# Kernel optimization log

Measured on AMD Instinct MI355X. Metric: run time of the kernel, lower is better.

The kernel has to match this reference:

```python
import jax, jax.numpy as jnp
import numpy as np
from jax import lax

B, L = 2, 5000            # images, candidate lines per image
C_IN, C_LOI = 256, 128    # backbone channels, dim_loi
H = W = 256               # feature-map spatial size (indices clamped to 255)
N_PTS0, N_PTS1 = 32, 8    # points sampled per line, after maxpool
POOL = N_PTS0 // N_PTS1   # MaxPool1d kernel/stride = 4
PLANES = C_LOI // 2       # Bottleneck1D mid channels
EPS = 1e-5


def setup_inputs() -> dict:
    key = jax.random.key(0)
    ks = jax.random.split(key, 16)
    f32 = jnp.float32
    s = 0.05
    feature = jax.random.normal(ks[0], (B, C_IN, H, W), f32)
    lines = jax.random.uniform(ks[1], (B, L, 2, 2), f32, minval=0.0, maxval=255.0)
    return {
        "feature": feature,
        "lines": lines,
        "fc1_w": jax.random.normal(ks[2], (C_LOI, C_IN), f32) * s,
        "fc1_b": jnp.zeros((C_LOI,), f32),
        "bn1_g": jnp.ones((C_LOI,), f32),
        "bn1_b": jnp.zeros((C_LOI,), f32),
        "bn1_m": jax.random.normal(ks[3], (C_LOI,), f32) * 0.1,
        "bn1_v": jax.random.uniform(ks[4], (C_LOI,), f32, minval=0.5, maxval=1.5),
        "conv1_w": jax.random.normal(ks[5], (PLANES, C_LOI), f32) * s,
        "conv1_b": jnp.zeros((PLANES,), f32),
        "bn2_g": jnp.ones((PLANES,), f32),
        "bn2_b": jnp.zeros((PLANES,), f32),
        "bn2_m": jax.random.normal(ks[6], (PLANES,), f32) * 0.1,
        "bn2_v": jax.random.uniform(ks[7], (PLANES,), f32, minval=0.5, maxval=1.5),
        "conv2_w": jax.random.normal(ks[8], (PLANES, PLANES, 3), f32) * s,
        "conv2_b": jnp.zeros((PLANES,), f32),
        "bn3_g": jnp.ones((PLANES,), f32),
        "bn3_b": jnp.zeros((PLANES,), f32),
        "bn3_m": jax.random.normal(ks[9], (PLANES,), f32) * 0.1,
        "bn3_v": jax.random.uniform(ks[10], (PLANES,), f32, minval=0.5, maxval=1.5),
        "conv3_w": jax.random.normal(ks[11], (C_LOI, PLANES), f32) * s,
        "conv3_b": jnp.zeros((C_LOI,), f32),
        "fc2_w": jax.random.normal(ks[12], (3, C_LOI * N_PTS1), f32) * s,
        "fc2_b": jnp.zeros((3,), f32),
    }


def _bn(x, g, b, m, v):
    # eval-mode BatchNorm1d over [N, C, T]
    inv = g / jnp.sqrt(v + EPS)
    return x * inv[None, :, None] + (b - m * inv)[None, :, None]


def _bilinear_sample(feat, lines):
    # feat: [B, C, H, W], lines: [B, L, 2, 2] -> [B, L, C, N_PTS0]
    lam = jnp.linspace(0.0, 1.0, N_PTS0, dtype=feat.dtype)[:, None]  # [P,1]
    # p = lam * endpoint0 + (1-lam) * endpoint1 - 0.5  -> [B, L, P, 2]
    p = lines[:, :, 0:1, :] * lam + lines[:, :, 1:2, :] * (1.0 - lam) - 0.5
    px, py = p[..., 0], p[..., 1]                       # [B, L, P]
    px0 = jnp.clip(jnp.floor(px), 0.0, 255.0)
    py0 = jnp.clip(jnp.floor(py), 0.0, 255.0)
    px1 = jnp.clip(px0 + 1.0, 0.0, 255.0)
    py1 = jnp.clip(py0 + 1.0, 0.0, 255.0)
    ix0, iy0 = px0.astype(jnp.int32), py0.astype(jnp.int32)
    ix1, iy1 = px1.astype(jnp.int32), py1.astype(jnp.int32)
    w00 = (px1 - px) * (py1 - py)
    w10 = (px - px0) * (py1 - py)
    w01 = (px1 - px) * (py - py0)
    w11 = (px - px0) * (py - py0)

    def one_image(f, a0, b0, a1, b1, c00, c10, c01, c11):
        # f: [C,H,W], indices/weights: [L,P] -> [C,L,P]
        return (f[:, a0, b0] * c00 + f[:, a1, b0] * c10 +
                f[:, a0, b1] * c01 + f[:, a1, b1] * c11)

    xp = jax.vmap(one_image)(feat, ix0, iy0, ix1, iy1, w00, w10, w01, w11)
    return jnp.transpose(xp, (0, 2, 1, 3))  # [B, L, C, P]


def _forward(feature, lines, fc1_w, fc1_b, bn1_g, bn1_b, bn1_m, bn1_v,
             conv1_w, conv1_b, bn2_g, bn2_b, bn2_m, bn2_v,
             conv2_w, conv2_b, bn3_g, bn3_b, bn3_m, bn3_v,
             conv3_w, conv3_b, fc2_w, fc2_b):
    # fc1: 1x1 conv over the backbone feature map
    x = jnp.einsum('oc,bchw->bohw', fc1_w, feature) + fc1_b[None, :, None, None]
    xp = _bilinear_sample(x, lines)                     # [B, L, C_LOI, P]
    xp = xp.reshape(B * L, C_LOI, N_PTS0)
    # MaxPool1d(kernel=POOL, stride=POOL)
    xp = xp.reshape(B * L, C_LOI, N_PTS1, POOL).max(axis=-1)  # [N, C, T]
    # Bottleneck1D residual branch: BN-ReLU-Conv1(k1)-BN-ReLU-Conv(k3)-BN-ReLU-Conv(k1)
    h = jax.nn.relu(_bn(xp, bn1_g, bn1_b, bn1_m, bn1_v))
    h = jnp.einsum('oc,nct->not', conv1_w, h) + conv1_b[None, :, None]
    h = jax.nn.relu(_bn(h, bn2_g, bn2_b, bn2_m, bn2_v))
    h = lax.conv_general_dilated(h, conv2_w, window_strides=(1,),
                                 padding=((1, 1),),
                                 dimension_numbers=('NCH', 'OIH', 'NCH'))
    h = h + conv2_b[None, :, None]
    h = jax.nn.relu(_bn(h, bn3_g, bn3_b, bn3_m, bn3_v))
    h = jnp.einsum('oc,nct->not', conv3_w, h) + conv3_b[None, :, None]
    xp = xp + h
    # fc2: ReLU + Linear(dim_loi * n_pts1 -> 3)
    flat = jax.nn.relu(xp).reshape(B * L, C_LOI * N_PTS1)
    return flat @ fc2_w.T + fc2_b


def reference(feature, lines, fc1_w, fc1_b, bn1_g, bn1_b, bn1_m, bn1_v,
              conv1_w, conv1_b, bn2_g, bn2_b, bn2_m, bn2_v,
              conv2_w, conv2_b, bn3_g, bn3_b, bn3_m, bn3_v,
              conv3_w, conv3_b, fc2_w, fc2_b):
    return _forward(feature, lines, fc1_w, fc1_b, bn1_g, bn1_b, bn1_m, bn1_v,
                    conv1_w, conv1_b, bn2_g, bn2_b, bn2_m, bn2_v,
                    conv2_w, conv2_b, bn3_g, bn3_b, bn3_m, bn3_v,
                    conv3_w, conv3_b, fc2_w, fc2_b)
```

## Files before the change

### kernel.cpp

```cpp
#include <hip/hip_runtime.h>
#include <hip/hip_bf16.h>

#define BB 2
#define LL 5000
#define CIN 256
#define CLOI 128
#define HH 256
#define WW 256
#define HWP (HH*WW)
#define NPTS0 32
#define NPTS1 8
#define PLANES 64
#define EPSV 1e-5f

#define X_BYTES   ((size_t)BB * HWP * CLOI * 2)
#define XS_BYTES  ((size_t)BB * LL * 1024 * 2)
#define W1S_OFF   (X_BYTES + XS_BYTES)
#define W2S_OFF   (W1S_OFF + 16384)
#define W3S_OFF   (W2S_OFF + 24576)
#define B1P_OFF   (W3S_OFF + 16384)
#define B2P_OFF   (B1P_OFF + 256)
#define S1_OFF    (B2P_OFF + 256)
#define T1_OFF    (S1_OFF + 512)
#define W0S_OFF   (T1_OFF + 512)

typedef unsigned int uint;
typedef unsigned short ushort;
typedef __attribute__((ext_vector_type(8))) short short8;
typedef __attribute__((ext_vector_type(4))) float f32x4;

__device__ __forceinline__ float bf2f(ushort u) {
    uint v = ((uint)u) << 16;
    return __uint_as_float(v);
}
__device__ __forceinline__ ushort f2bf(float f) {
    uint x = __float_as_uint(f);
    uint r = (x + 0x7fffu + ((x >> 16) & 1u)) >> 16;
    return (ushort)r;
}
__device__ __forceinline__ uint pack2(float a, float b) {
    return (uint)f2bf(a) | ((uint)f2bf(b) << 16);
}

__global__ __launch_bounds__(256) void fc1_kernel(
    const float* __restrict__ feature, const ushort* __restrict__ w0s,
    const float* __restrict__ fc1_b, ushort* __restrict__ xout)
{
    __shared__ ushort sF[32 * 64 * 8];

    int tid = threadIdx.x;
    int tile = blockIdx.x;
    int b = tile >> 10;
    int p0 = (tile & 1023) << 6;
    int wv = tid >> 6, lane = tid & 63;
    int q = lane >> 4, ln = lane & 15;

    short8 afr[8][2];
#pragma unroll
    for (int kg = 0; kg < 8; kg++)
#pragma unroll
        for (int mt = 0; mt < 2; mt++)
            afr[kg][mt] = *(const short8*)(w0s + ((size_t)((kg * 4 + q) * 128 + wv * 32 + mt * 16 + ln)) * 8);

    const float* fb = feature + (size_t)b * CIN * HWP + p0;
    int g_ = tid >> 4;
    int qd = tid & 15;
#pragma unroll
    for (int s = 0; s < 2; s++) {
        int g = s * 16 + g_;
        const float* src = fb + (size_t)(g * 8) * HWP + qd * 4;
        float4 rv[8];
#pragma unroll
        for (int j = 0; j < 8; j++) rv[j] = *(const float4*)(src + (size_t)j * HWP);
#pragma unroll
        for (int i = 0; i < 4; i++) {
            uint4 u;
            u.x = pack2(((const float*)&rv[0])[i], ((const float*)&rv[1])[i]);
            u.y = pack2(((const float*)&rv[2])[i], ((const float*)&rv[3])[i]);
            u.z = pack2(((const float*)&rv[4])[i], ((const float*)&rv[5])[i]);
            u.w = pack2(((const float*)&rv[6])[i], ((const float*)&rv[7])[i]);
            *(uint4*)(&sF[(g * 64 + qd * 4 + i) * 8]) = u;
        }
    }
    __syncthreads();

    const f32x4 fzero = { 0.f, 0.f, 0.f, 0.f };
    f32x4 acc[2][4];
#pragma unroll
    for (int mt = 0; mt < 2; mt++)
#pragma unroll
        for (int nt = 0; nt < 4; nt++) acc[mt][nt] = fzero;

#pragma unroll
    for (int kg = 0; kg < 8; kg++) {
#pragma unroll
        for (int nt = 0; nt < 4; nt++) {
            short8 bfr = *(short8*)(&sF[((kg * 4 + q) * 64 + nt * 16 + ln) * 8]);
            acc[0][nt] = __builtin_amdgcn_mfma_f32_16x16x32_bf16(afr[kg][0], bfr, acc[0][nt], 0, 0, 0);
            acc[1][nt] = __builtin_amdgcn_mfma_f32_16x16x32_bf16(afr[kg][1], bfr, acc[1][nt], 0, 0, 0);
        }
    }

    float bias[8];
    *(float4*)bias       = *(const float4*)(fc1_b + wv * 32 + q * 4);
    *(float4*)(bias + 4) = *(const float4*)(fc1_b + wv * 32 + 16 + q * 4);
    ushort* xrow = xout + (size_t)b * HWP * CLOI;
#pragma unroll
    for (int mt = 0; mt < 2; mt++)
#pragma unroll
        for (int nt = 0; nt < 4; nt++) {
            uint2 u;
            u.x = pack2(acc[mt][nt][0] + bias[mt * 4 + 0], acc[mt][nt][1] + bias[mt * 4 + 1]);
            u.y = pack2(acc[mt][nt][2] + bias[mt * 4 + 2], acc[mt][nt][3] + bias[mt * 4 + 3]);
            *(uint2*)(xrow + (size_t)(p0 + nt * 16 + ln) * CLOI + wv * 32 + mt * 16 + q * 4) = u;
        }
}

__global__ __launch_bounds__(256) void prep_kernel(
    const float* __restrict__ conv1_w, const float* __restrict__ conv1_b,
    const float* __restrict__ bn2_g, const float* __restrict__ bn2_b,
    const float* __restrict__ bn2_m, const float* __restrict__ bn2_v,
    const float* __restrict__ conv2_w, const float* __restrict__ conv2_b,
    const float* __restrict__ bn3_g, const float* __restrict__ bn3_b,
    const float* __restrict__ bn3_m, const float* __restrict__ bn3_v,
    const float* __restrict__ conv3_w,
    const float* __restrict__ bn1_g, const float* __restrict__ bn1_b,
    const float* __restrict__ bn1_m, const float* __restrict__ bn1_v,
    const float* __restrict__ fc1_w,
    ushort* __restrict__ w1s, ushort* __restrict__ w2s, ushort* __restrict__ w3s,
    float* __restrict__ b1p, float* __restrict__ b2p,
    float* __restrict__ s1o, float* __restrict__ t1o,
    ushort* __restrict__ w0s)
{
    int idx = blockIdx.x * 256 + threadIdx.x;
    if (idx < 8192) {
        int kg = idx >> 9, rem = idx & 511, m = rem >> 3, j = rem & 7;
        int c = kg * 8 + j;
        float s2 = bn2_g[m] * rsqrtf(bn2_v[m] + EPSV);
        w1s[idx] = f2bf(conv1_w[m * 128 + c] * s2);
    }
    if (idx < 12288) {
        int dt = idx >> 12, rem = idx & 4095;
        int kg = rem >> 9, m = (rem >> 3) & 63, j = rem & 7;
        int i = kg * 8 + j;
        float s3 = bn3_g[m] * rsqrtf(bn3_v[m] + EPSV);
        w2s[idx] = f2bf(conv2_w[m * 192 + i * 3 + dt] * s3);
    }
    if (idx < 8192) {
        int kg = idx >> 10, rem = idx & 1023, m = rem >> 3, j = rem & 7;
        w3s[idx] = f2bf(conv3_w[m * 64 + kg * 8 + j]);
    }
    if (idx < 32768) {
        int grp = idx >> 10, rem = idx & 1023, m = rem >> 3, j = rem & 7;
        w0s[idx] = f2bf(fc1_w[m * CIN + grp * 8 + j]);
    }
    if (idx < 64) {
        float s2 = bn2_g[idx] * rsqrtf(bn2_v[idx] + EPSV);
        b1p[idx] = conv1_b[idx] * s2 + bn2_b[idx] - bn2_m[idx] * s2;
        float s3 = bn3_g[idx] * rsqrtf(bn3_v[idx] + EPSV);
        b2p[idx] = conv2_b[idx] * s3 + bn3_b[idx] - bn3_m[idx] * s3;
    }
    if (idx < 128) {
        float s1 = bn1_g[idx] * rsqrtf(bn1_v[idx] + EPSV);
        s1o[idx] = s1;
        t1o[idx] = bn1_b[idx] - bn1_m[idx] * s1;
    }
}

__global__ __launch_bounds__(256, 5) void sample_head_kernel(
    const ushort* __restrict__ x, const float* __restrict__ lines,
    const ushort* __restrict__ w1s, const ushort* __restrict__ w2s,
    const ushort* __restrict__ w3s,
    const float* __restrict__ b1p, const float* __restrict__ b2p,
    const float* __restrict__ s1g, const float* __restrict__ t1g,
    const float* __restrict__ conv3_b,
    const float* __restrict__ fc2_w, const float* __restrict__ fc2_b,
    float* __restrict__ out)
{
    __shared__ ushort sH1[8192];
    __shared__ __align__(16) char sU[8192];
    __shared__ float sB1[64], sB2b[64], sB3b[128];

    int*    sI  = (int*)sU;
    float2* sW2 = (float2*)(sU + 1024);
    ushort* sB2 = (ushort*)sU;

    int tid = threadIdx.x;
    int wv = tid >> 6, lane = tid & 63;
    int q = lane >> 4, ln = lane & 15;
    int L0 = blockIdx.x * 8;
    int b = L0 / LL;
    int colg = wv * 16 + ln;

    if (tid < 128) sB3b[tid] = conv3_b[tid];
    if (tid < 64)  { sB1[tid] = b1p[tid]; sB2b[tid] = b2p[tid]; }

    int half = lane >> 5;
    int lc = lane & 31;
    int kg = lc >> 1, j4 = (lc & 1) * 4;
    int swz = (kg & 7) << 3;

    float4 s1v = *(const float4*)(s1g + lc * 4);
    float4 t1v = *(const float4*)(t1g + lc * 4);

    {
        int l = tid >> 5, j = tid & 31;
        float lam = (float)j * (1.0f / 31.0f);
        const float* lp = lines + (size_t)(L0 + l) * 4;
        float e0x = lp[0], e0y = lp[1], e1x = lp[2], e1y = lp[3];
        float px = e0x * lam + e1x * (1.f - lam) - 0.5f;
        float py = e0y * lam + e1y * (1.f - lam) - 0.5f;
        float px0 = fminf(fmaxf(floorf(px), 0.f), 255.f);
        float py0 = fminf(fmaxf(floorf(py), 0.f), 255.f);
        int ix0 = (int)px0, iy0 = (int)py0;
        sI[l * 32 + j] = ix0 * WW + iy0;
        float2 w2; w2.x = px0 + 1.f - px; w2.y = py0 + 1.f - py;
        sW2[l * 32 + j] = w2;
    }
    __syncthreads();

    const uint2* xb2 = (const uint2*)(x + (size_t)b * HWP * CLOI);

    uint2 xsu[8];
#pragma unroll
    for (int l = 0; l < 8; l++) {
        uint2 u[4][4];
        float2 wxy[4];
#pragma unroll
        for (int jj = 0; jj < 4; jj++) {
            int pt = l * 32 + wv * 8 + half * 4 + jj;
            int i00 = sI[pt];
            wxy[jj] = sW2[pt];
            const uint2* rp = xb2 + (size_t)((i00 << 5) + lc);
            u[jj][0] = rp[0];
            u[jj][1] = rp[32];
            u[jj][2] = rp[8192];
            u[jj][3] = rp[8224];
        }
        float p0v = -INFINITY, p1v = -INFINITY, p2v = -INFINITY, p3v = -INFINITY;
#pragma unroll
        for (int jj = 0; jj < 4; jj++) {
            float wx0 = wxy[jj].x, wy0 = wxy[jj].y;
            float w00 = wx0 * wy0;
            float w01 = wx0 - w00;
            float w10 = wy0 - w00;
            float w11 = 1.f - wx0 - wy0 + w00;
            float v0 = bf2f((ushort)(u[jj][0].x & 0xffff)) * w00 + bf2f((ushort)(u[jj][1].x & 0xffff)) * w01
                     + bf2f((ushort)(u[jj][2].x & 0xffff)) * w10 + bf2f((ushort)(u[jj][3].x & 0xffff)) * w11;
            float v1 = bf2f((ushort)(u[jj][0].x >> 16)) * w00 + bf2f((ushort)(u[jj][1].x >> 16)) * w01
                     + bf2f((ushort)(u[jj][2].x >> 16)) * w10 + bf2f((ushort)(u[jj][3].x >> 16)) * w11;
            float v2 = bf2f((ushort)(u[jj][0].y & 0xffff)) * w00 + bf2f((ushort)(u[jj][1].y & 0xffff)) * w01
                     + bf2f((ushort)(u[jj][2].y & 0xffff)) * w10 + bf2f((ushort)(u[jj][3].y & 0xffff)) * w11;
            float v3 = bf2f((ushort)(u[jj][0].y >> 16)) * w00 + bf2f((ushort)(u[jj][1].y >> 16)) * w01
                     + bf2f((ushort)(u[jj][2].y >> 16)) * w10 + bf2f((ushort)(u[jj][3].y >> 16)) * w11;
            p0v = fmaxf(p0v, v0); p1v = fmaxf(p1v, v1);
            p2v = fmaxf(p2v, v2); p3v = fmaxf(p3v, v3);
        }
        uint2 xv; xv.x = pack2(p0v, p1v); xv.y = pack2(p2v, p3v);
        xsu[l] = xv;
        float h0 = fmaxf(p0v * s1v.x + t1v.x, 0.f);
        float h1v = fmaxf(p1v * s1v.y + t1v.y, 0.f);
        float h2 = fmaxf(p2v * s1v.z + t1v.z, 0.f);
        float h3 = fmaxf(p3v * s1v.w + t1v.w, 0.f);
        uint2 hv; hv.x = pack2(h0, h1v); hv.y = pack2(h2, h3);
        int col = l * 8 + 2 * wv + half;
        int base = (kg * 64 + col) * 8 + j4;
        *(uint2*)(&sH1[base ^ swz]) = hv;
    }
    __syncthreads();

    const short8 bzero = { 0, 0, 0, 0, 0, 0, 0, 0 };
    const f32x4 fzero = { 0.f, 0.f, 0.f, 0.f };

    f32x4 acc1[4];
#pragma unroll
    for (int mt = 0; mt < 4; mt++) acc1[mt] = fzero;
#pragma unroll
    for (int ks = 0; ks < 4; ks++) {
        int kk = ks * 4 + q;
        short8 bfrag = *(short8*)(&sH1[((kk * 64 + colg) * 8) ^ ((kk & 7) << 3)]);
#pragma unroll
        for (int mt = 0; mt < 4; mt++) {
            short8 a = *(const short8*)(w1s + (kk * 64 + mt * 16 + ln) * 8);
            acc1[mt] = __builtin_amdgcn_mfma_f32_16x16x32_bf16(a, bfrag, acc1[mt], 0, 0, 0);
        }
    }
#pragma unroll
    for (int mt = 0; mt < 4; mt++) {
        int m0 = mt * 16 + q * 4;
        float v0 = fmaxf(acc1[mt][0] + sB1[m0 + 0], 0.f);
        float v1 = fmaxf(acc1[mt][1] + sB1[m0 + 1], 0.f);
        float v2 = fmaxf(acc1[mt][2] + sB1[m0 + 2], 0.f);
        float v3 = fmaxf(acc1[mt][3] + sB1[m0 + 3], 0.f);
        uint2 u; u.x = pack2(v0, v1); u.y = pack2(v2, v3);
        *(uint2*)(&sB2[((m0 >> 3) * 64 + colg) * 8 + (m0 & 7)]) = u;
    }
    __syncthreads();

#pragma unroll
    for (int l = 0; l < 8; l++) {
        int col = l * 8 + 2 * wv + half;
        int base = (kg * 64 + col) * 8 + j4;
        *(uint2*)(&sH1[base ^ swz]) = xsu[l];
    }

    int tpos = colg & 7;
    short8 bfr2[3][2];
#pragma unroll
    for (int dt = 0; dt < 3; dt++) {
        int tsh = tpos + dt - 1;
        bool valid = ((unsigned)tsh < 8u);
        int colr = colg + dt - 1;
        colr = colr < 0 ? 0 : (colr > 63 ? 63 : colr);
#pragma unroll
        for (int ks = 0; ks < 2; ks++) {
            short8 bfrag = *(short8*)(&sB2[((ks * 4 + q) * 64 + colr) * 8]);
            bfr2[dt][ks] = valid ? bfrag : bzero;
        }
    }
    __syncthreads();

    f32x4 acc2[4];
#pragma unroll
    for (int mt = 0; mt < 4; mt++) acc2[mt] = fzero;
#pragma unroll
    for (int dt = 0; dt < 3; dt++)
#pragma unroll
        for (int ks = 0; ks < 2; ks++) {
            int kk = ks * 4 + q;
#pragma unroll
            for (int mt = 0; mt < 4; mt++) {
                short8 a = *(const short8*)(w2s + dt * 4096 + (kk * 64 + mt * 16 + ln) * 8);
                acc2[mt] = __builtin_amdgcn_mfma_f32_16x16x32_bf16(a, bfr2[dt][ks], acc2[mt], 0, 0, 0);
            }
        }
#pragma unroll
    for (int mt = 0; mt < 4; mt++) {
        int m0 = mt * 16 + q * 4;
        float v0 = fmaxf(acc2[mt][0] + sB2b[m0 + 0], 0.f);
        float v1 = fmaxf(acc2[mt][1] + sB2b[m0 + 1], 0.f);
        float v2 = fmaxf(acc2[mt][2] + sB2b[m0 + 2], 0.f);
        float v3 = fmaxf(acc2[mt][3] + sB2b[m0 + 3], 0.f);
        uint2 u; u.x = pack2(v0, v1); u.y = pack2(v2, v3);
        *(uint2*)(&sB2[((m0 >> 3) * 64 + colg) * 8 + (m0 & 7)]) = u;
    }
    __syncthreads();

    f32x4 acc3[8];
#pragma unroll
    for (int mt = 0; mt < 8; mt++) acc3[mt] = fzero;
#pragma unroll
    for (int ks = 0; ks < 2; ks++) {
        int kk = ks * 4 + q;
        short8 bfrag = *(short8*)(&sB2[(kk * 64 + colg) * 8]);
#pragma unroll
        for (int mt = 0; mt < 8; mt++) {
            short8 a = *(const short8*)(w3s + (kk * 128 + mt * 16 + ln) * 8);
            acc3[mt] = __builtin_amdgcn_mfma_f32_16x16x32_bf16(a, bfrag, acc3[mt], 0, 0, 0);
        }
    }

    float p0 = 0.f, p1 = 0.f, p2 = 0.f;
#pragma unroll
    for (int mt = 0; mt < 8; mt++) {
#pragma unroll
        for (int r = 0; r < 4; r++) {
            int m = mt * 16 + q * 4 + r;
            int idx = ((m >> 3) * 512 + colg * 8 + (m & 7)) ^ (((m >> 3) & 7) << 3);
            float xsv = bf2f(sH1[idx]);
            float v = fmaxf(xsv + acc3[mt][r] + sB3b[m], 0.f);
            int fi = m * 8 + tpos;
            p0 += v * fc2_w[fi];
            p1 += v * fc2_w[1024 + fi];
            p2 += v * fc2_w[2048 + fi];
        }
    }
    p0 += __shfl_xor(p0, 32); p1 += __shfl_xor(p1, 32); p2 += __shfl_xor(p2, 32);
    p0 += __shfl_xor(p0, 16); p1 += __shfl_xor(p1, 16); p2 += __shfl_xor(p2, 16);
    p0 += __shfl_xor(p0, 4);  p1 += __shfl_xor(p1, 4);  p2 += __shfl_xor(p2, 4);
    p0 += __shfl_xor(p0, 2);  p1 += __shfl_xor(p1, 2);  p2 += __shfl_xor(p2, 2);
    p0 += __shfl_xor(p0, 1);  p1 += __shfl_xor(p1, 1);  p2 += __shfl_xor(p2, 1);

    if (lane == 0 || lane == 8) {
        int line = L0 + wv * 2 + (lane >> 3);
        out[(size_t)line * 3 + 0] = p0 + fc2_b[0];
        out[(size_t)line * 3 + 1] = p1 + fc2_b[1];
        out[(size_t)line * 3 + 2] = p2 + fc2_b[2];
    }
}

extern "C" void kernel_launch(void* const* d_in, const int* in_sizes, int n_in,
                              void* d_out, int out_size, void* d_ws, size_t ws_size,
                              hipStream_t stream) {
    const float* feature = (const float*)d_in[0];
    const float* lines   = (const float*)d_in[1];
    const float* fc1_w   = (const float*)d_in[2];
    const float* fc1_b   = (const float*)d_in[3];
    const float* bn1_g   = (const float*)d_in[4];
    const float* bn1_b   = (const float*)d_in[5];
    const float* bn1_m   = (const float*)d_in[6];
    const float* bn1_v   = (const float*)d_in[7];
    const float* conv1_w = (const float*)d_in[8];
    const float* conv1_b = (const float*)d_in[9];
    const float* bn2_g   = (const float*)d_in[10];
    const float* bn2_b   = (const float*)d_in[11];
    const float* bn2_m   = (const float*)d_in[12];
    const float* bn2_v   = (const float*)d_in[13];
    const float* conv2_w = (const float*)d_in[14];
    const float* conv2_b = (const float*)d_in[15];
    const float* bn3_g   = (const float*)d_in[16];
    const float* bn3_b   = (const float*)d_in[17];
    const float* bn3_m   = (const float*)d_in[18];
    const float* bn3_v   = (const float*)d_in[19];
    const float* conv3_w = (const float*)d_in[20];
    const float* conv3_b = (const float*)d_in[21];
    const float* fc2_w   = (const float*)d_in[22];
    const float* fc2_b   = (const float*)d_in[23];
    float* out = (float*)d_out;

    char* ws = (char*)d_ws;
    ushort* x_bf = (ushort*)ws;
    ushort* w1s  = (ushort*)(ws + W1S_OFF);
    ushort* w2s  = (ushort*)(ws + W2S_OFF);
    ushort* w3s  = (ushort*)(ws + W3S_OFF);
    float*  b1p  = (float*)(ws + B1P_OFF);
    float*  b2p  = (float*)(ws + B2P_OFF);
    float*  s1g  = (float*)(ws + S1_OFF);
    float*  t1g  = (float*)(ws + T1_OFF);
    ushort* w0s  = (ushort*)(ws + W0S_OFF);

    prep_kernel<<<128, 256, 0, stream>>>(
        conv1_w, conv1_b, bn2_g, bn2_b, bn2_m, bn2_v,
        conv2_w, conv2_b, bn3_g, bn3_b, bn3_m, bn3_v,
        conv3_w, bn1_g, bn1_b, bn1_m, bn1_v, fc1_w,
        w1s, w2s, w3s, b1p, b2p, s1g, t1g, w0s);
    fc1_kernel<<<2048, 256, 0, stream>>>(feature, w0s, fc1_b, x_bf);
    sample_head_kernel<<<BB * LL / 8, 256, 0, stream>>>(
        x_bf, lines, w1s, w2s, w3s, b1p, b2p, s1g, t1g, conv3_b, fc2_w, fc2_b, out);
}
```

Measured before the change: 290.0 us.

## Store pooled features to LDS and apply BN1+ReLU at MFMA fragment load

The gather loop now writes the max-pooled bf16 features straight into shared memory and drops the per-thread xsu[8] register array. The BN1 scale/shift and ReLU are applied when the conv1 B-fragments are read, with the scale and shift vectors staged in shared memory. The loop also issues gathers for two lines at a time, putting 32 loads in flight per thread. This cuts long-lived registers and removes the later re-store of xsu, but adds bf16 unpack/repack work and extra LDS reads in the MFMA stage. The BN input is also rounded to bf16 before scaling, which changes numerics slightly.

Measured after the change: 288.1 us. No clear change (-0.6%).

```diff
diff --git a/kernel.cpp b/kernel.cpp
--- a/kernel.cpp
+++ b/kernel.cpp
@@ -179,6 +179,7 @@
 {
     __shared__ ushort sH1[8192];
     __shared__ __align__(16) char sU[8192];
+    __shared__ float sS1[128], sT1[128];
     __shared__ float sB1[64], sB2b[64], sB3b[128];
 
     int*    sI  = (int*)sU;
@@ -192,16 +193,13 @@
     int b = L0 / LL;
     int colg = wv * 16 + ln;
 
-    if (tid < 128) sB3b[tid] = conv3_b[tid];
+    if (tid < 128) { sB3b[tid] = conv3_b[tid]; sS1[tid] = s1g[tid]; sT1[tid] = t1g[tid]; }
     if (tid < 64)  { sB1[tid] = b1p[tid]; sB2b[tid] = b2p[tid]; }
 
     int half = lane >> 5;
     int lc = lane & 31;
     int kg = lc >> 1, j4 = (lc & 1) * 4;
     int swz = (kg & 7) << 3;
-
-    float4 s1v = *(const float4*)(s1g + lc * 4);
-    float4 t1v = *(const float4*)(t1g + lc * 4);
 
     {
         int l = tid >> 5, j = tid & 31;
@@ -221,51 +219,50 @@
 
     const uint2* xb2 = (const uint2*)(x + (size_t)b * HWP * CLOI);
 
-    uint2 xsu[8];
-#pragma unroll
-    for (int l = 0; l < 8; l++) {
-        uint2 u[4][4];
-        float2 wxy[4];
-#pragma unroll
-        for (int jj = 0; jj < 4; jj++) {
-            int pt = l * 32 + wv * 8 + half * 4 + jj;
-            int i00 = sI[pt];
-            wxy[jj] = sW2[pt];
-            const uint2* rp = xb2 + (size_t)((i00 << 5) + lc);
-            u[jj][0] = rp[0];
-            u[jj][1] = rp[32];
-            u[jj][2] = rp[8192];
-            u[jj][3] = rp[8224];
-        }
-        float p0v = -INFINITY, p1v = -INFINITY, p2v = -INFINITY, p3v = -INFINITY;
-#pragma unroll
-        for (int jj = 0; jj < 4; jj++) {
-            float wx0 = wxy[jj].x, wy0 = wxy[jj].y;
-            float w00 = wx0 * wy0;
-            float w01 = wx0 - w00;
-            float w10 = wy0 - w00;
-            float w11 = 1.f - wx0 - wy0 + w00;
-            float v0 = bf2f((ushort)(u[jj][0].x & 0xffff)) * w00 + bf2f((ushort)(u[jj][1].x & 0xffff)) * w01
-                     + bf2f((ushort)(u[jj][2].x & 0xffff)) * w10 + bf2f((ushort)(u[jj][3].x & 0xffff)) * w11;
-            float v1 = bf2f((ushort)(u[jj][0].x >> 16)) * w00 + bf2f((ushort)(u[jj][1].x >> 16)) * w01
-                     + bf2f((ushort)(u[jj][2].x >> 16)) * w10 + bf2f((ushort)(u[jj][3].x >> 16)) * w11;
-            float v2 = bf2f((ushort)(u[jj][0].y & 0xffff)) * w00 + bf2f((ushort)(u[jj][1].y & 0xffff)) * w01
-                     + bf2f((ushort)(u[jj][2].y & 0xffff)) * w10 + bf2f((ushort)(u[jj][3].y & 0xffff)) * w11;
-            float v3 = bf2f((ushort)(u[jj][0].y >> 16)) * w00 + bf2f((ushort)(u[jj][1].y >> 16)) * w01
-                     + bf2f((ushort)(u[jj][2].y >> 16)) * w10 + bf2f((ushort)(u[jj][3].y >> 16)) * w11;
-            p0v = fmaxf(p0v, v0); p1v = fmaxf(p1v, v1);
-            p2v = fmaxf(p2v, v2); p3v = fmaxf(p3v, v3);
-        }
-        uint2 xv; xv.x = pack2(p0v, p1v); xv.y = pack2(p2v, p3v);
-        xsu[l] = xv;
-        float h0 = fmaxf(p0v * s1v.x + t1v.x, 0.f);
-        float h1v = fmaxf(p1v * s1v.y + t1v.y, 0.f);
-        float h2 = fmaxf(p2v * s1v.z + t1v.z, 0.f);
-        float h3 = fmaxf(p3v * s1v.w + t1v.w, 0.f);
-        uint2 hv; hv.x = pack2(h0, h1v); hv.y = pack2(h2, h3);
-        int col = l * 8 + 2 * wv + half;
-        int base = (kg * 64 + col) * 8 + j4;
-        *(uint2*)(&sH1[base ^ swz]) = hv;
+#pragma unroll
+    for (int lp = 0; lp < 4; lp++) {
+        uint2 u[2][4][4];
+        float2 wxy[2][4];
+#pragma unroll
+        for (int h2 = 0; h2 < 2; h2++) {
+#pragma unroll
+            for (int jj = 0; jj < 4; jj++) {
+                int pt = (lp * 2 + h2) * 32 + wv * 8 + half * 4 + jj;
+                int i00 = sI[pt];
+                wxy[h2][jj] = sW2[pt];
+                const uint2* rp = xb2 + (size_t)((i00 << 5) + lc);
+                u[h2][jj][0] = rp[0];
+                u[h2][jj][1] = rp[32];
+                u[h2][jj][2] = rp[8192];
+                u[h2][jj][3] = rp[8224];
+            }
+        }
+#pragma unroll
+        for (int h2 = 0; h2 < 2; h2++) {
+            float p0v = -INFINITY, p1v = -INFINITY, p2v = -INFINITY, p3v = -INFINITY;
+#pragma unroll
+            for (int jj = 0; jj < 4; jj++) {
+                float wx0 = wxy[h2][jj].x, wy0 = wxy[h2][jj].y;
+                float w00 = wx0 * wy0;
+                float w01 = wx0 - w00;
+                float w10 = wy0 - w00;
+                float w11 = 1.f - wx0 - wy0 + w00;
+                float v0 = bf2f((ushort)(u[h2][jj][0].x & 0xffff)) * w00 + bf2f((ushort)(u[h2][jj][1].x & 0xffff)) * w01
+                         + bf2f((ushort)(u[h2][jj][2].x & 0xffff)) * w10 + bf2f((ushort)(u[h2][jj][3].x & 0xffff)) * w11;
+                float v1 = bf2f((ushort)(u[h2][jj][0].x >> 16)) * w00 + bf2f((ushort)(u[h2][jj][1].x >> 16)) * w01
+                         + bf2f((ushort)(u[h2][jj][2].x >> 16)) * w10 + bf2f((ushort)(u[h2][jj][3].x >> 16)) * w11;
+                float v2 = bf2f((ushort)(u[h2][jj][0].y & 0xffff)) * w00 + bf2f((ushort)(u[h2][jj][1].y & 0xffff)) * w01
+                         + bf2f((ushort)(u[h2][jj][2].y & 0xffff)) * w10 + bf2f((ushort)(u[h2][jj][3].y & 0xffff)) * w11;
+                float v3 = bf2f((ushort)(u[h2][jj][0].y >> 16)) * w00 + bf2f((ushort)(u[h2][jj][1].y >> 16)) * w01
+                         + bf2f((ushort)(u[h2][jj][2].y >> 16)) * w10 + bf2f((ushort)(u[h2][jj][3].y >> 16)) * w11;
+                p0v = fmaxf(p0v, v0); p1v = fmaxf(p1v, v1);
+                p2v = fmaxf(p2v, v2); p3v = fmaxf(p3v, v3);
+            }
+            uint2 xv; xv.x = pack2(p0v, p1v); xv.y = pack2(p2v, p3v);
+            int col = (lp * 2 + h2) * 8 + 2 * wv + half;
+            int base = (kg * 64 + col) * 8 + j4;
+            *(uint2*)(&sH1[base ^ swz]) = xv;
+        }
     }
     __syncthreads();
 
@@ -278,7 +275,21 @@
 #pragma unroll
     for (int ks = 0; ks < 4; ks++) {
         int kk = ks * 4 + q;
-        short8 bfrag = *(short8*)(&sH1[((kk * 64 + colg) * 8) ^ ((kk & 7) << 3)]);
+        short8 xf = *(short8*)(&sH1[((kk * 64 + colg) * 8) ^ ((kk & 7) << 3)]);
+        float s1r[8], t1r[8];
+        *(float4*)(s1r)     = *(const float4*)(&sS1[kk * 8]);
+        *(float4*)(s1r + 4) = *(const float4*)(&sS1[kk * 8 + 4]);
+        *(float4*)(t1r)     = *(const float4*)(&sT1[kk * 8]);
+        *(float4*)(t1r + 4) = *(const float4*)(&sT1[kk * 8 + 4]);
+        uint hw[4];
+#pragma unroll
+        for (int p = 0; p < 4; p++) {
+            float a = fmaxf(bf2f((ushort)xf[2 * p])     * s1r[2 * p]     + t1r[2 * p], 0.f);
+            float c = fmaxf(bf2f((ushort)xf[2 * p + 1]) * s1r[2 * p + 1] + t1r[2 * p + 1], 0.f);
+            hw[p] = pack2(a, c);
+        }
+        uint4 hv4; hv4.x = hw[0]; hv4.y = hw[1]; hv4.z = hw[2]; hv4.w = hw[3];
+        short8 bfrag = *(short8*)&hv4;
 #pragma unroll
         for (int mt = 0; mt < 4; mt++) {
             short8 a = *(const short8*)(w1s + (kk * 64 + mt * 16 + ln) * 8);
@@ -296,13 +307,6 @@
         *(uint2*)(&sB2[((m0 >> 3) * 64 + colg) * 8 + (m0 & 7)]) = u;
     }
     __syncthreads();
-
-#pragma unroll
-    for (int l = 0; l < 8; l++) {
-        int col = l * 8 + 2 * wv + half;
-        int base = (kg * 64 + col) * 8 + j4;
-        *(uint2*)(&sH1[base ^ swz]) = xsu[l];
-    }
 
     int tpos = colg & 7;
     short8 bfr2[3][2];
```
